# Kernel optimization log

Measured on AMD Instinct MI355X. Metric: run time of the kernel, lower is better.

## Reference

```python
import jax, jax.numpy as jnp
import numpy as np

NB_HEAD = 8
SIZE_PER_HEAD = 32
KEY_SIZE = 32
RATE = 2


def extract_seq_patches(x, kernel_size, rate):
    # x: [B, N, d] -> [B, N, kernel_size, d], dilated local windows (stride=rate)
    B, N, d = x.shape
    k_size = kernel_size + (rate - 1) * (kernel_size - 1)
    p_right = (k_size - 1) // 2
    p_left = k_size - 1 - p_right
    xp = jnp.pad(x, ((0, 0), (p_left, p_right), (0, 0)))
    xs = [xp[:, i:i + N] for i in range(0, k_size, rate)]  # kernel_size slices
    return jnp.stack(xs, axis=2)


def setup_inputs() -> dict:
    key = jax.random.key(0)
    k1, k2, k3 = jax.random.split(key, 3)
    B, S, D = 4, 2046, 256
    x = jax.random.normal(k1, (B, S, D), dtype=jnp.float32)
    # scale like nn.Linear init so softmax logits are well-conditioned
    W = jax.random.normal(k2, (D, NB_HEAD * SIZE_PER_HEAD), dtype=jnp.float32) / np.sqrt(D)
    b = jax.random.normal(k3, (NB_HEAD * SIZE_PER_HEAD,), dtype=jnp.float32) * 0.01
    return {"x": x, "W": W, "b": b}


def reference(x, W, b):
    rate, heads, dk, dv = RATE, NB_HEAD, KEY_SIZE, SIZE_PER_HEAD
    B, S, D = x.shape
    pad_len = rate - S % rate
    xp = jnp.pad(x, ((0, 0), (0, pad_len), (0, 0)))
    N = S + pad_len
    m = N // rate
    qkv = xp @ W + b                 # same Linear used for Q, K, V in the original
    Q = K = V = qkv                  # [B, N, heads*dk]
    ksz = 1 + 2 * (rate - 1)
    kwp = extract_seq_patches(K, ksz, rate)   # [B, N, ksz, H*dk]
    vwp = extract_seq_patches(V, ksz, rate)
    qw = Q.reshape(B, m, rate, heads, dk).transpose(0, 3, 2, 1, 4)   # [B,H,r,m,dk]
    kw = K.reshape(B, m, rate, heads, dk).transpose(0, 3, 2, 1, 4)
    vw = V.reshape(B, m, rate, heads, dv).transpose(0, 3, 2, 1, 4)
    kwp = kwp.reshape(B, m, rate, ksz, heads, dk).transpose(0, 4, 2, 1, 3, 5)  # [B,H,r,m,ksz,dk]
    vwp = vwp.reshape(B, m, rate, ksz, heads, dv).transpose(0, 4, 2, 1, 3, 5)
    scale = 1.0 / np.sqrt(dk).astype(np.float32)
    # strided scores; original transposes the last two dims (a.permute(0,1,2,4,3))
    a = jnp.einsum('bhrid,bhrjd->bhrji', qw, kw) * scale             # [B,H,r,m,m]
    # local-window scores: qw (as length-1 query) against dilated patches
    ap = jnp.einsum('bhrid,bhrikd->bhrik', qw, kwp) * scale          # [B,H,r,m,ksz]
    A = jax.nn.softmax(jnp.concatenate([a, ap], axis=-1), axis=-1)
    a, ap = A[..., :m], A[..., m:]
    o1 = jnp.einsum('bhrij,bhrjd->bhrid', a, vw)                     # [B,H,r,m,dv]
    o2 = jnp.einsum('bhrik,bhrikd->bhrid', ap, vwp)
    o = (o1 + o2).transpose(0, 3, 2, 1, 4).reshape(B, N, heads * dv)
    return o[:, :-pad_len]
```

## Files before the change

### kernel.cpp

```cpp
#include <hip/hip_runtime.h>
#include <stdint.h>
#include <stddef.h>

#define NB_HEAD 8
#define DHEAD   32
#define B_      4
#define S_      2046
#define N_      2048
#define M_      1024
#define D_      256

typedef __attribute__((ext_vector_type(8))) short short8;
typedef __attribute__((ext_vector_type(4))) float f32x4;

__device__ __forceinline__ void bf2x2(uint32_t u, float& lo, float& hi) {
    union { uint32_t i; float f; } a, b;
    a.i = u << 16;
    b.i = u & 0xffff0000u;
    lo = a.f; hi = b.f;
}
__device__ __forceinline__ float bf2f(uint16_t u) {
    union { uint32_t i; float f; } v; v.i = ((uint32_t)u) << 16; return v.f;
}
__device__ __forceinline__ uint16_t f2bf(float f) {
    union { float f; uint32_t i; } v; v.f = f;
    uint32_t u = v.i;
    u += 0x7fffu + ((u >> 16) & 1u);
    return (uint16_t)(u >> 16);
}
__device__ __forceinline__ short8 ld_frag(const uint16_t* p) {
    union { uint4 u; short8 s; } v;
    v.u = *(const uint4*)p;
    return v.s;
}
__device__ __forceinline__ void unp8(short8 v, float* f) {
    union { short8 s; uint32_t u[4]; } x; x.s = v;
    #pragma unroll
    for (int k = 0; k < 4; ++k) bf2x2(x.u[k], f[2*k], f[2*k+1]);
}
__device__ __forceinline__ uint32_t pkbf(uint32_t hi, uint32_t lo) {
    return __builtin_amdgcn_perm(hi, lo, 0x07060302u);
}

__global__ __launch_bounds__(256) void wt_kernel(
    const float* __restrict__ W, uint16_t* __restrict__ Wt)
{
    const int t  = blockIdx.x * 256 + threadIdx.x;
    const int c  = t >> 6;
    const int k0 = (t & 63) * 4;
    union { uint16_t h[4]; uint2 u; } v;
    #pragma unroll
    for (int kk = 0; kk < 4; ++kk)
        v.h[kk] = f2bf(W[(size_t)(k0 + kk) * D_ + c]);
    *(uint2*)(Wt + (size_t)c * D_ + k0) = v.u;
}

__global__ __launch_bounds__(256) void proj_kernel(
    const float* __restrict__ x, const uint16_t* __restrict__ Wt,
    const float* __restrict__ bias,
    uint16_t* __restrict__ qkv, uint16_t* __restrict__ qkvT)
{
    __shared__ uint16_t Tl[64 * 80];
    const int tid  = threadIdx.x;
    const int w    = tid >> 6;
    const int lane = tid & 63;
    const int q    = lane >> 4;
    const int n16  = lane & 15;
    const int rg   = blockIdx.x >> 2;
    const int cg   = blockIdx.x & 3;
    const int n0   = rg * 64;
    const int b    = n0 >> 11;
    const int nnb  = n0 & 2047;
    const int c0   = cg * 64;

    const f32x4 kZ = {0.f, 0.f, 0.f, 0.f};
    f32x4 acc[4];
    #pragma unroll
    for (int nt = 0; nt < 4; ++nt) acc[nt] = kZ;

    const int nrow = nnb + w * 16 + n16;
    const bool ok  = (nrow < S_);
    const float* xrow = x + ((size_t)b * S_ + (ok ? nrow : 0)) * D_;

    #pragma unroll
    for (int kc = 0; kc < 8; ++kc) {
        short8 A;
        if (ok) {
            const uint32_t* xp2 = (const uint32_t*)(xrow + kc * 32 + q * 8);
            uint4 f0 = *(const uint4*)xp2;
            uint4 f1 = *(const uint4*)(xp2 + 4);
            union { uint32_t u[4]; short8 s; } av;
            av.u[0] = pkbf(f0.y + 0x8000u, f0.x + 0x8000u);
            av.u[1] = pkbf(f0.w + 0x8000u, f0.z + 0x8000u);
            av.u[2] = pkbf(f1.y + 0x8000u, f1.x + 0x8000u);
            av.u[3] = pkbf(f1.w + 0x8000u, f1.z + 0x8000u);
            A = av.s;
        } else {
            A = short8{0,0,0,0,0,0,0,0};
        }
        #pragma unroll
        for (int nt = 0; nt < 4; ++nt) {
            short8 Bf = ld_frag(Wt + (size_t)(c0 + nt * 16 + n16) * D_ + kc * 32 + q * 8);
            acc[nt] = __builtin_amdgcn_mfma_f32_16x16x32_bf16(A, Bf, acc[nt], 0, 0, 0);
        }
    }

    #pragma unroll
    for (int nt = 0; nt < 4; ++nt) {
        const float bv = bias[c0 + nt * 16 + n16];
        #pragma unroll
        for (int r = 0; r < 4; ++r)
            Tl[(w * 16 + q * 4 + r) * 80 + nt * 16 + n16] = f2bf(acc[nt][r] + bv);
    }
    __syncthreads();

    const int hloc = w >> 1, rr = w & 1;
    const int hglob = (c0 >> 5) + hloc;
    const int pglob = (b * NB_HEAD + hglob) * 2 + rr;
    const int ibase = nnb >> 1;
    uint16_t* qk = qkv  + (size_t)pglob * (M_ * DHEAD);
    uint16_t* qt = qkvT + (size_t)pglob * (M_ * DHEAD);

    {
        const int ii = lane >> 1, d0 = (lane & 1) * 16;
        const uint4* src = (const uint4*)(Tl + (2 * ii + rr) * 80 + hloc * 32 + d0);
        uint4 v0 = src[0], v1 = src[1];
        uint4* dst = (uint4*)(qk + (size_t)(ibase + ii) * DHEAD + d0);
        dst[0] = v0; dst[1] = v1;
    }
    {
        const int d = lane >> 1, ph = (lane & 1) * 16;
        uint32_t pk[8];
        #pragma unroll
        for (int t = 0; t < 16; ++t) {
            const int pos = ph + t;
            const int il = (((pos >> 2) & 1) << 4) | (((pos >> 3) & 3) << 2) | (pos & 3);
            const uint32_t vv = Tl[(2 * il + rr) * 80 + hloc * 32 + d];
            if (t & 1) pk[t >> 1] |= vv << 16; else pk[t >> 1] = vv;
        }
        uint4* dst = (uint4*)(qt + (size_t)d * M_ + ibase + ph);
        dst[0] = *(uint4*)&pk[0];
        dst[1] = *(uint4*)&pk[4];
    }
}

__global__ __launch_bounds__(256) void attn_kernel(
    const uint16_t* __restrict__ qkv, const uint16_t* __restrict__ qkvT,
    float* __restrict__ out)
{
    const float SCL = 0.17677669529663687f * 1.4426950408889634f;
    const int tid  = threadIdx.x;
    const int w    = tid >> 6;
    const int lane = tid & 63;
    const int q    = lane >> 4;
    const int n16  = lane & 15;
    const int bid  = blockIdx.x;
    const int p     = ((bid & 7) << 3) | ((bid >> 3) & 7);
    const int chunk = bid >> 6;
    const uint16_t* Xp = qkv  + (size_t)p * (M_ * DHEAD);
    const uint16_t* Xt = qkvT + (size_t)p * (M_ * DHEAD);

    const int rbase = chunk * 128 + w * 32;
    const f32x4 kZ = {0.f, 0.f, 0.f, 0.f};

    short8 Q0 = ld_frag(Xp + (size_t)(rbase + n16) * DHEAD + q * 8);
    short8 Q1 = ld_frag(Xp + (size_t)(rbase + 16 + n16) * DHEAD + q * 8);

    f32x4 Ot[2][2];
    #pragma unroll
    for (int it = 0; it < 2; ++it) { Ot[it][0] = kZ; Ot[it][1] = kZ; }
    float Lp[2] = {0.f, 0.f};

    short8 Bf[4], XF[2][2];
    #pragma unroll
    for (int g = 0; g < 4; ++g)
        Bf[g] = ld_frag(Xp + (size_t)(g * 16 + n16) * DHEAD + q * 8);
    #pragma unroll
    for (int h = 0; h < 2; ++h)
        #pragma unroll
        for (int c = 0; c < 2; ++c)
            XF[h][c] = ld_frag(Xt + (size_t)(h * 16 + n16) * M_ + c * 32 + q * 8);

    for (int tile = 0; tile < 16; ++tile) {
        f32x4 S0[4], S1[4];
        #pragma unroll
        for (int g = 0; g < 4; ++g) {
            S0[g] = __builtin_amdgcn_mfma_f32_16x16x32_bf16(Bf[g], Q0, kZ, 0, 0, 0);
            S1[g] = __builtin_amdgcn_mfma_f32_16x16x32_bf16(Bf[g], Q1, kZ, 0, 0, 0);
        }
        const int jb2 = ((tile + 1) & 15) * 64;
        short8 Bn[4], XFn[2][2];
        #pragma unroll
        for (int g = 0; g < 4; ++g)
            Bn[g] = ld_frag(Xp + (size_t)(jb2 + g * 16 + n16) * DHEAD + q * 8);
        #pragma unroll
        for (int h = 0; h < 2; ++h)
            #pragma unroll
            for (int c = 0; c < 2; ++c)
                XFn[h][c] = ld_frag(Xt + (size_t)(h * 16 + n16) * M_ + jb2 + c * 32 + q * 8);

        #pragma unroll
        for (int it = 0; it < 2; ++it) {
            f32x4* S = it ? S1 : S0;
            uint32_t t[4][4];
            float rs = 0.f;
            #pragma unroll
            for (int g = 0; g < 4; ++g)
                #pragma unroll
                for (int r = 0; r < 4; ++r) {
                    float e = exp2f(S[g][r] * SCL);
                    uint32_t tt = (__float_as_uint(e) + 0x8000u) & 0xffff0000u;
                    t[g][r] = tt;
                    rs += __uint_as_float(tt);
                }
            Lp[it] += rs;
            #pragma unroll
            for (int c = 0; c < 2; ++c) {
                union { uint32_t u[4]; short8 s; } bp;
                bp.u[0] = pkbf(t[2*c][1],   t[2*c][0]);
                bp.u[1] = pkbf(t[2*c][3],   t[2*c][2]);
                bp.u[2] = pkbf(t[2*c+1][1], t[2*c+1][0]);
                bp.u[3] = pkbf(t[2*c+1][3], t[2*c+1][2]);
                Ot[it][0] = __builtin_amdgcn_mfma_f32_16x16x32_bf16(XF[0][c], bp.s, Ot[it][0], 0, 0, 0);
                Ot[it][1] = __builtin_amdgcn_mfma_f32_16x16x32_bf16(XF[1][c], bp.s, Ot[it][1], 0, 0, 0);
            }
        }
        #pragma unroll
        for (int g = 0; g < 4; ++g) Bf[g] = Bn[g];
        #pragma unroll
        for (int h = 0; h < 2; ++h) {
            XF[h][0] = XFn[h][0]; XF[h][1] = XFn[h][1];
        }
    }

    #pragma unroll
    for (int it = 0; it < 2; ++it) {
        Lp[it] += __shfl_xor(Lp[it], 16, 64);
        Lp[it] += __shfl_xor(Lp[it], 32, 64);
    }

    const int rpar  = p & 1;
    const int hh    = (p >> 1) & 7;
    const int bglob = p >> 4;

    #pragma unroll
    for (int it = 0; it < 2; ++it) {
        const int i = rbase + it * 16 + n16;
        float qf[8];
        unp8(it ? Q1 : Q0, qf);
        const int im1 = max(i - 1, 0);
        const int ip1 = min(i + 1, M_ - 1);

        float fm[8], fp[8];
        unp8(ld_frag(Xp + (size_t)im1 * DHEAD + q * 8), fm);
        unp8(ld_frag(Xp + (size_t)ip1 * DHEAD + q * 8), fp);
        float sm = 0.f, s0 = 0.f, sp = 0.f;
        #pragma unroll
        for (int jj = 0; jj < 8; ++jj) {
            sm = fmaf(qf[jj], fm[jj], sm);
            s0 = fmaf(qf[jj], qf[jj], s0);
            sp = fmaf(qf[jj], fp[jj], sp);
        }
        sm += __shfl_xor(sm, 16, 64); sm += __shfl_xor(sm, 32, 64);
        s0 += __shfl_xor(s0, 16, 64); s0 += __shfl_xor(s0, 32, 64);
        sp += __shfl_xor(sp, 16, 64); sp += __shfl_xor(sp, 32, 64);

        const bool vOK = (i > 0), wOK = (i < M_ - 1);
        const float em = vOK ? exp2f(sm * SCL) : 1.0f;
        const float e0 = exp2f(s0 * SCL);
        const float ep = wOK ? exp2f(sp * SCL) : 1.0f;
        const float vm = vOK ? em : 0.f;
        const float vp = wOK ? ep : 0.f;
        const float inv = 1.0f / (Lp[it] + em + e0 + ep);

        if (i < M_ - 1) {
            const size_t rowb = ((size_t)bglob * S_ + 2 * i + rpar) * D_ + hh * DHEAD;
            #pragma unroll
            for (int h = 0; h < 2; ++h) {
                float xm[4], x0[4], xp4[4];
                {
                    uint2 u = *(const uint2*)(Xp + (size_t)im1 * DHEAD + h * 16 + q * 4);
                    bf2x2(u.x, xm[0], xm[1]); bf2x2(u.y, xm[2], xm[3]);
                }
                {
                    uint2 u = *(const uint2*)(Xp + (size_t)i * DHEAD + h * 16 + q * 4);
                    bf2x2(u.x, x0[0], x0[1]); bf2x2(u.y, x0[2], x0[3]);
                }
                {
                    uint2 u = *(const uint2*)(Xp + (size_t)ip1 * DHEAD + h * 16 + q * 4);
                    bf2x2(u.x, xp4[0], xp4[1]); bf2x2(u.y, xp4[2], xp4[3]);
                }
                float4 res;
                #pragma unroll
                for (int r = 0; r < 4; ++r) {
                    float v = Ot[it][h][r] + vm * xm[r] + e0 * x0[r] + vp * xp4[r];
                    ((float*)&res)[r] = v * inv;
                }
                *(float4*)(out + rowb + h * 16 + q * 4) = res;
            }
        }
    }
}

extern "C" void kernel_launch(void* const* d_in, const int* in_sizes, int n_in,
                              void* d_out, int out_size, void* d_ws, size_t ws_size,
                              hipStream_t stream) {
    const float* x    = (const float*)d_in[0];
    const float* W    = (const float*)d_in[1];
    const float* bias = (const float*)d_in[2];
    uint16_t* qkv  = (uint16_t*)d_ws;
    uint16_t* qkvT = (uint16_t*)d_ws + (size_t)64 * M_ * DHEAD;
    uint16_t* Wt   = qkvT + (size_t)64 * M_ * DHEAD;
    float* out = (float*)d_out;

    hipLaunchKernelGGL(wt_kernel,   dim3(64),  dim3(256), 0, stream, W, Wt);
    hipLaunchKernelGGL(proj_kernel, dim3(512), dim3(256), 0, stream,
                       x, Wt, bias, qkv, qkvT);
    hipLaunchKernelGGL(attn_kernel, dim3(512), dim3(256), 0, stream,
                       qkv, qkvT, out);
}
```

Before: 106.9 us.

## Halve per-block work in projection and attention kernels to double grid size

```diff
diff --git a/kernel.cpp b/kernel.cpp
--- a/kernel.cpp
+++ b/kernel.cpp
@@ -60,23 +60,22 @@
     const float* __restrict__ bias,
     uint16_t* __restrict__ qkv, uint16_t* __restrict__ qkvT)
 {
-    __shared__ uint16_t Tl[64 * 80];
+    __shared__ uint16_t Tl[64 * 40];
     const int tid  = threadIdx.x;
     const int w    = tid >> 6;
     const int lane = tid & 63;
     const int q    = lane >> 4;
     const int n16  = lane & 15;
-    const int rg   = blockIdx.x >> 2;
-    const int cg   = blockIdx.x & 3;
+    const int rg   = blockIdx.x >> 3;
+    const int cg   = blockIdx.x & 7;
     const int n0   = rg * 64;
     const int b    = n0 >> 11;
     const int nnb  = n0 & 2047;
-    const int c0   = cg * 64;
+    const int c0   = cg * 32;
 
     const f32x4 kZ = {0.f, 0.f, 0.f, 0.f};
-    f32x4 acc[4];
-    #pragma unroll
-    for (int nt = 0; nt < 4; ++nt) acc[nt] = kZ;
+    f32x4 acc[2];
+    acc[0] = kZ; acc[1] = kZ;
 
     const int nrow = nnb + w * 16 + n16;
     const bool ok  = (nrow < S_);
@@ -99,48 +98,46 @@
             A = short8{0,0,0,0,0,0,0,0};
         }
         #pragma unroll
-        for (int nt = 0; nt < 4; ++nt) {
+        for (int nt = 0; nt < 2; ++nt) {
             short8 Bf = ld_frag(Wt + (size_t)(c0 + nt * 16 + n16) * D_ + kc * 32 + q * 8);
             acc[nt] = __builtin_amdgcn_mfma_f32_16x16x32_bf16(A, Bf, acc[nt], 0, 0, 0);
         }
     }
 
     #pragma unroll
-    for (int nt = 0; nt < 4; ++nt) {
+    for (int nt = 0; nt < 2; ++nt) {
         const float bv = bias[c0 + nt * 16 + n16];
         #pragma unroll
         for (int r = 0; r < 4; ++r)
-            Tl[(w * 16 + q * 4 + r) * 80 + nt * 16 + n16] = f2bf(acc[nt][r] + bv);
+            Tl[(w * 16 + q * 4 + r) * 40 + nt * 16 + n16] = f2bf(acc[nt][r] + bv);
     }
     __syncthreads();
 
-    const int hloc = w >> 1, rr = w & 1;
-    const int hglob = (c0 >> 5) + hloc;
-    const int pglob = (b * NB_HEAD + hglob) * 2 + rr;
+    const int rr   = w & 1;
+    const int half = w >> 1;
+    const int pglob = (b * NB_HEAD + cg) * 2 + rr;
     const int ibase = nnb >> 1;
     uint16_t* qk = qkv  + (size_t)pglob * (M_ * DHEAD);
     uint16_t* qt = qkvT + (size_t)pglob * (M_ * DHEAD);
 
     {
-        const int ii = lane >> 1, d0 = (lane & 1) * 16;
-        const uint4* src = (const uint4*)(Tl + (2 * ii + rr) * 80 + hloc * 32 + d0);
-        uint4 v0 = src[0], v1 = src[1];
-        uint4* dst = (uint4*)(qk + (size_t)(ibase + ii) * DHEAD + d0);
-        dst[0] = v0; dst[1] = v1;
+        const int il = half * 16 + (lane >> 2);
+        const int d0 = (lane & 3) * 8;
+        uint4 v = *(const uint4*)(Tl + (2 * il + rr) * 40 + d0);
+        *(uint4*)(qk + (size_t)(ibase + il) * DHEAD + d0) = v;
     }
     {
-        const int d = lane >> 1, ph = (lane & 1) * 16;
-        uint32_t pk[8];
-        #pragma unroll
-        for (int t = 0; t < 16; ++t) {
-            const int pos = ph + t;
+        const int d  = half * 16 + (lane >> 2);
+        const int p0 = (lane & 3) * 8;
+        uint32_t pk[4];
+        #pragma unroll
+        for (int t = 0; t < 8; ++t) {
+            const int pos = p0 + t;
             const int il = (((pos >> 2) & 1) << 4) | (((pos >> 3) & 3) << 2) | (pos & 3);
-            const uint32_t vv = Tl[(2 * il + rr) * 80 + hloc * 32 + d];
+            const uint32_t vv = Tl[(2 * il + rr) * 40 + d];
             if (t & 1) pk[t >> 1] |= vv << 16; else pk[t >> 1] = vv;
         }
-        uint4* dst = (uint4*)(qt + (size_t)d * M_ + ibase + ph);
-        dst[0] = *(uint4*)&pk[0];
-        dst[1] = *(uint4*)&pk[4];
+        *(uint4*)(qt + (size_t)d * M_ + ibase + p0) = *(uint4*)&pk[0];
     }
 }
 
@@ -160,16 +157,14 @@
     const uint16_t* Xp = qkv  + (size_t)p * (M_ * DHEAD);
     const uint16_t* Xt = qkvT + (size_t)p * (M_ * DHEAD);
 
-    const int rbase = chunk * 128 + w * 32;
+    const int rbase = chunk * 64 + w * 16;
     const f32x4 kZ = {0.f, 0.f, 0.f, 0.f};
 
     short8 Q0 = ld_frag(Xp + (size_t)(rbase + n16) * DHEAD + q * 8);
-    short8 Q1 = ld_frag(Xp + (size_t)(rbase + 16 + n16) * DHEAD + q * 8);
-
-    f32x4 Ot[2][2];
-    #pragma unroll
-    for (int it = 0; it < 2; ++it) { Ot[it][0] = kZ; Ot[it][1] = kZ; }
-    float Lp[2] = {0.f, 0.f};
+
+    f32x4 Ot[2];
+    Ot[0] = kZ; Ot[1] = kZ;
+    float Lp = 0.f;
 
     short8 Bf[4], XF[2][2];
     #pragma unroll
@@ -182,12 +177,11 @@
             XF[h][c] = ld_frag(Xt + (size_t)(h * 16 + n16) * M_ + c * 32 + q * 8);
 
     for (int tile = 0; tile < 16; ++tile) {
-        f32x4 S0[4], S1[4];
-        #pragma unroll
-        for (int g = 0; g < 4; ++g) {
-            S0[g] = __builtin_amdgcn_mfma_f32_16x16x32_bf16(Bf[g], Q0, kZ, 0, 0, 0);
-            S1[g] = __builtin_amdgcn_mfma_f32_16x16x32_bf16(Bf[g], Q1, kZ, 0, 0, 0);
-        }
+        f32x4 S[4];
+        #pragma unroll
+        for (int g = 0; g < 4; ++g)
+            S[g] = __builtin_amdgcn_mfma_f32_16x16x32_bf16(Bf[g], Q0, kZ, 0, 0, 0);
+
         const int jb2 = ((tile + 1) & 15) * 64;
         short8 Bn[4], XFn[2][2];
         #pragma unroll
@@ -199,31 +193,26 @@
             for (int c = 0; c < 2; ++c)
                 XFn[h][c] = ld_frag(Xt + (size_t)(h * 16 + n16) * M_ + jb2 + c * 32 + q * 8);
 
-        #pragma unroll
-        for (int it = 0; it < 2; ++it) {
-            f32x4* S = it ? S1 : S0;
-            uint32_t t[4][4];
-            float rs = 0.f;
+        uint32_t t[4][4];
+        float rs = 0.f;
+        #pragma unroll
+        for (int g = 0; g < 4; ++g)
             #pragma unroll
-            for (int g = 0; g < 4; ++g)
-                #pragma unroll
-                for (int r = 0; r < 4; ++r) {
-                    float e = exp2f(S[g][r] * SCL);
-                    uint32_t tt = (__float_as_uint(e) + 0x8000u) & 0xffff0000u;
-                    t[g][r] = tt;
-                    rs += __uint_as_float(tt);
-                }
-            Lp[it] += rs;
-            #pragma unroll
-            for (int c = 0; c < 2; ++c) {
-                union { uint32_t u[4]; short8 s; } bp;
-                bp.u[0] = pkbf(t[2*c][1],   t[2*c][0]);
-                bp.u[1] = pkbf(t[2*c][3],   t[2*c][2]);
-                bp.u[2] = pkbf(t[2*c+1][1], t[2*c+1][0]);
-                bp.u[3] = pkbf(t[2*c+1][3], t[2*c+1][2]);
-                Ot[it][0] = __builtin_amdgcn_mfma_f32_16x16x32_bf16(XF[0][c], bp.s, Ot[it][0], 0, 0, 0);
-                Ot[it][1] = __builtin_amdgcn_mfma_f32_16x16x32_bf16(XF[1][c], bp.s, Ot[it][1], 0, 0, 0);
+            for (int r = 0; r < 4; ++r) {
+                float e = exp2f(S[g][r] * SCL);
+                t[g][r] = __float_as_uint(e) + 0x8000u;
+                rs += e;
             }
+        Lp += rs;
+        #pragma unroll
+        for (int c = 0; c < 2; ++c) {
+            union { uint32_t u[4]; short8 s; } bp;
+            bp.u[0] = pkbf(t[2*c][1],   t[2*c][0]);
+            bp.u[1] = pkbf(t[2*c][3],   t[2*c][2]);
+            bp.u[2] = pkbf(t[2*c+1][1], t[2*c+1][0]);
+            bp.u[3] = pkbf(t[2*c+1][3], t[2*c+1][2]);
+            Ot[0] = __builtin_amdgcn_mfma_f32_16x16x32_bf16(XF[0][c], bp.s, Ot[0], 0, 0, 0);
+            Ot[1] = __builtin_amdgcn_mfma_f32_16x16x32_bf16(XF[1][c], bp.s, Ot[1], 0, 0, 0);
         }
         #pragma unroll
         for (int g = 0; g < 4; ++g) Bf[g] = Bn[g];
@@ -233,21 +222,17 @@
         }
     }
 
-    #pragma unroll
-    for (int it = 0; it < 2; ++it) {
-        Lp[it] += __shfl_xor(Lp[it], 16, 64);
-        Lp[it] += __shfl_xor(Lp[it], 32, 64);
-    }
+    Lp += __shfl_xor(Lp, 16, 64);
+    Lp += __shfl_xor(Lp, 32, 64);
 
     const int rpar  = p & 1;
     const int hh    = (p >> 1) & 7;
     const int bglob = p >> 4;
 
-    #pragma unroll
-    for (int it = 0; it < 2; ++it) {
-        const int i = rbase + it * 16 + n16;
+    {
+        const int i = rbase + n16;
         float qf[8];
-        unp8(it ? Q1 : Q0, qf);
+        unp8(Q0, qf);
         const int im1 = max(i - 1, 0);
         const int ip1 = min(i + 1, M_ - 1);
 
@@ -271,7 +256,7 @@
         const float ep = wOK ? exp2f(sp * SCL) : 1.0f;
         const float vm = vOK ? em : 0.f;
         const float vp = wOK ? ep : 0.f;
-        const float inv = 1.0f / (Lp[it] + em + e0 + ep);
+        const float inv = 1.0f / (Lp + em + e0 + ep);
 
         if (i < M_ - 1) {
             const size_t rowb = ((size_t)bglob * S_ + 2 * i + rpar) * D_ + hh * DHEAD;
@@ -293,7 +278,7 @@
                 float4 res;
                 #pragma unroll
                 for (int r = 0; r < 4; ++r) {
-                    float v = Ot[it][h][r] + vm * xm[r] + e0 * x0[r] + vp * xp4[r];
+                    float v = Ot[h][r] + vm * xm[r] + e0 * x0[r] + vp * xp4[r];
                     ((float*)&res)[r] = v * inv;
                 }
                 *(float4*)(out + rowb + h * 16 + q * 4) = res;
@@ -313,9 +298,9 @@
     uint16_t* Wt   = qkvT + (size_t)64 * M_ * DHEAD;
     float* out = (float*)d_out;
 
-    hipLaunchKernelGGL(wt_kernel,   dim3(64),  dim3(256), 0, stream, W, Wt);
-    hipLaunchKernelGGL(proj_kernel, dim3(512), dim3(256), 0, stream,
+    hipLaunchKernelGGL(wt_kernel,   dim3(64),   dim3(256), 0, stream, W, Wt);
+    hipLaunchKernelGGL(proj_kernel, dim3(1024), dim3(256), 0, stream,
                        x, Wt, bias, qkv, qkvT);
-    hipLaunchKernelGGL(attn_kernel, dim3(512), dim3(256), 0, stream,
+    hipLaunchKernelGGL(attn_kernel, dim3(1024), dim3(256), 0, stream,
                        qkv, qkvT, out);
 }
```

New measurement: 140.8 us. 1.32x slower.

## Split reduction dimension across two wave groups in projection and attention kernels

Applied to the files above, without the earlier changes.

```diff
diff --git a/kernel.cpp b/kernel.cpp
--- a/kernel.cpp
+++ b/kernel.cpp
@@ -55,17 +55,20 @@
     *(uint2*)(Wt + (size_t)c * D_ + k0) = v.u;
 }
 
-__global__ __launch_bounds__(256) void proj_kernel(
+__global__ __launch_bounds__(512) void proj_kernel(
     const float* __restrict__ x, const uint16_t* __restrict__ Wt,
     const float* __restrict__ bias,
     uint16_t* __restrict__ qkv, uint16_t* __restrict__ qkvT)
 {
+    __shared__ float    mrgP[4][16][64];
     __shared__ uint16_t Tl[64 * 80];
     const int tid  = threadIdx.x;
     const int w    = tid >> 6;
     const int lane = tid & 63;
     const int q    = lane >> 4;
     const int n16  = lane & 15;
+    const int rp   = w & 3;
+    const int kh   = w >> 2;
     const int rg   = blockIdx.x >> 2;
     const int cg   = blockIdx.x & 3;
     const int n0   = rg * 64;
@@ -78,15 +81,16 @@
     #pragma unroll
     for (int nt = 0; nt < 4; ++nt) acc[nt] = kZ;
 
-    const int nrow = nnb + w * 16 + n16;
+    const int nrow = nnb + rp * 16 + n16;
     const bool ok  = (nrow < S_);
     const float* xrow = x + ((size_t)b * S_ + (ok ? nrow : 0)) * D_;
 
     #pragma unroll
-    for (int kc = 0; kc < 8; ++kc) {
+    for (int kc = 0; kc < 4; ++kc) {
+        const int k0 = kh * 128 + kc * 32;
         short8 A;
         if (ok) {
-            const uint32_t* xp2 = (const uint32_t*)(xrow + kc * 32 + q * 8);
+            const uint32_t* xp2 = (const uint32_t*)(xrow + k0 + q * 8);
             uint4 f0 = *(const uint4*)xp2;
             uint4 f1 = *(const uint4*)(xp2 + 4);
             union { uint32_t u[4]; short8 s; } av;
@@ -100,67 +104,85 @@
         }
         #pragma unroll
         for (int nt = 0; nt < 4; ++nt) {
-            short8 Bf = ld_frag(Wt + (size_t)(c0 + nt * 16 + n16) * D_ + kc * 32 + q * 8);
+            short8 Bf = ld_frag(Wt + (size_t)(c0 + nt * 16 + n16) * D_ + k0 + q * 8);
             acc[nt] = __builtin_amdgcn_mfma_f32_16x16x32_bf16(A, Bf, acc[nt], 0, 0, 0);
         }
     }
 
-    #pragma unroll
-    for (int nt = 0; nt < 4; ++nt) {
-        const float bv = bias[c0 + nt * 16 + n16];
-        #pragma unroll
-        for (int r = 0; r < 4; ++r)
-            Tl[(w * 16 + q * 4 + r) * 80 + nt * 16 + n16] = f2bf(acc[nt][r] + bv);
+    if (kh == 1) {
+        #pragma unroll
+        for (int nt = 0; nt < 4; ++nt)
+            #pragma unroll
+            for (int r = 0; r < 4; ++r)
+                mrgP[rp][nt * 4 + r][lane] = acc[nt][r];
     }
     __syncthreads();
-
-    const int hloc = w >> 1, rr = w & 1;
-    const int hglob = (c0 >> 5) + hloc;
-    const int pglob = (b * NB_HEAD + hglob) * 2 + rr;
-    const int ibase = nnb >> 1;
-    uint16_t* qk = qkv  + (size_t)pglob * (M_ * DHEAD);
-    uint16_t* qt = qkvT + (size_t)pglob * (M_ * DHEAD);
-
-    {
-        const int ii = lane >> 1, d0 = (lane & 1) * 16;
-        const uint4* src = (const uint4*)(Tl + (2 * ii + rr) * 80 + hloc * 32 + d0);
-        uint4 v0 = src[0], v1 = src[1];
-        uint4* dst = (uint4*)(qk + (size_t)(ibase + ii) * DHEAD + d0);
-        dst[0] = v0; dst[1] = v1;
-    }
-    {
-        const int d = lane >> 1, ph = (lane & 1) * 16;
-        uint32_t pk[8];
-        #pragma unroll
-        for (int t = 0; t < 16; ++t) {
-            const int pos = ph + t;
-            const int il = (((pos >> 2) & 1) << 4) | (((pos >> 3) & 3) << 2) | (pos & 3);
-            const uint32_t vv = Tl[(2 * il + rr) * 80 + hloc * 32 + d];
-            if (t & 1) pk[t >> 1] |= vv << 16; else pk[t >> 1] = vv;
-        }
-        uint4* dst = (uint4*)(qt + (size_t)d * M_ + ibase + ph);
-        dst[0] = *(uint4*)&pk[0];
-        dst[1] = *(uint4*)&pk[4];
-    }
-}
-
-__global__ __launch_bounds__(256) void attn_kernel(
+    if (kh == 0) {
+        #pragma unroll
+        for (int nt = 0; nt < 4; ++nt) {
+            const float bv = bias[c0 + nt * 16 + n16];
+            #pragma unroll
+            for (int r = 0; r < 4; ++r) {
+                float v = acc[nt][r] + mrgP[rp][nt * 4 + r][lane] + bv;
+                Tl[(rp * 16 + q * 4 + r) * 80 + nt * 16 + n16] = f2bf(v);
+            }
+        }
+    }
+    __syncthreads();
+
+    if (w < 4) {
+        const int hloc = w >> 1, rr = w & 1;
+        const int hglob = (c0 >> 5) + hloc;
+        const int pglob = (b * NB_HEAD + hglob) * 2 + rr;
+        const int ibase = nnb >> 1;
+        uint16_t* qk = qkv  + (size_t)pglob * (M_ * DHEAD);
+        uint16_t* qt = qkvT + (size_t)pglob * (M_ * DHEAD);
+
+        {
+            const int ii = lane >> 1, d0 = (lane & 1) * 16;
+            const uint4* src = (const uint4*)(Tl + (2 * ii + rr) * 80 + hloc * 32 + d0);
+            uint4 v0 = src[0], v1 = src[1];
+            uint4* dst = (uint4*)(qk + (size_t)(ibase + ii) * DHEAD + d0);
+            dst[0] = v0; dst[1] = v1;
+        }
+        {
+            const int d = lane >> 1, ph = (lane & 1) * 16;
+            uint32_t pk[8];
+            #pragma unroll
+            for (int t = 0; t < 16; ++t) {
+                const int pos = ph + t;
+                const int il = (((pos >> 2) & 1) << 4) | (((pos >> 3) & 3) << 2) | (pos & 3);
+                const uint32_t vv = Tl[(2 * il + rr) * 80 + hloc * 32 + d];
+                if (t & 1) pk[t >> 1] |= vv << 16; else pk[t >> 1] = vv;
+            }
+            uint4* dst = (uint4*)(qt + (size_t)d * M_ + ibase + ph);
+            dst[0] = *(uint4*)&pk[0];
+            dst[1] = *(uint4*)&pk[4];
+        }
+    }
+}
+
+__global__ __launch_bounds__(512) void attn_kernel(
     const uint16_t* __restrict__ qkv, const uint16_t* __restrict__ qkvT,
     float* __restrict__ out)
 {
     const float SCL = 0.17677669529663687f * 1.4426950408889634f;
+    __shared__ float mrg[4][18][64];
     const int tid  = threadIdx.x;
     const int w    = tid >> 6;
     const int lane = tid & 63;
     const int q    = lane >> 4;
     const int n16  = lane & 15;
+    const int rowgrp = w & 3;
+    const int jh     = w >> 2;
     const int bid  = blockIdx.x;
     const int p     = ((bid & 7) << 3) | ((bid >> 3) & 7);
     const int chunk = bid >> 6;
     const uint16_t* Xp = qkv  + (size_t)p * (M_ * DHEAD);
     const uint16_t* Xt = qkvT + (size_t)p * (M_ * DHEAD);
 
-    const int rbase = chunk * 128 + w * 32;
+    const int rbase = chunk * 128 + rowgrp * 32;
+    const int jb0   = jh * 512;
     const f32x4 kZ = {0.f, 0.f, 0.f, 0.f};
 
     short8 Q0 = ld_frag(Xp + (size_t)(rbase + n16) * DHEAD + q * 8);
@@ -174,21 +196,21 @@
     short8 Bf[4], XF[2][2];
     #pragma unroll
     for (int g = 0; g < 4; ++g)
-        Bf[g] = ld_frag(Xp + (size_t)(g * 16 + n16) * DHEAD + q * 8);
+        Bf[g] = ld_frag(Xp + (size_t)(jb0 + g * 16 + n16) * DHEAD + q * 8);
     #pragma unroll
     for (int h = 0; h < 2; ++h)
         #pragma unroll
         for (int c = 0; c < 2; ++c)
-            XF[h][c] = ld_frag(Xt + (size_t)(h * 16 + n16) * M_ + c * 32 + q * 8);
-
-    for (int tile = 0; tile < 16; ++tile) {
+            XF[h][c] = ld_frag(Xt + (size_t)(h * 16 + n16) * M_ + jb0 + c * 32 + q * 8);
+
+    for (int tile = 0; tile < 8; ++tile) {
         f32x4 S0[4], S1[4];
         #pragma unroll
         for (int g = 0; g < 4; ++g) {
             S0[g] = __builtin_amdgcn_mfma_f32_16x16x32_bf16(Bf[g], Q0, kZ, 0, 0, 0);
             S1[g] = __builtin_amdgcn_mfma_f32_16x16x32_bf16(Bf[g], Q1, kZ, 0, 0, 0);
         }
-        const int jb2 = ((tile + 1) & 15) * 64;
+        const int jb2 = jb0 + ((tile + 1) & 7) * 64;
         short8 Bn[4], XFn[2][2];
         #pragma unroll
         for (int g = 0; g < 4; ++g)
@@ -237,6 +259,30 @@
     for (int it = 0; it < 2; ++it) {
         Lp[it] += __shfl_xor(Lp[it], 16, 64);
         Lp[it] += __shfl_xor(Lp[it], 32, 64);
+    }
+
+    if (jh == 1) {
+        #pragma unroll
+        for (int it = 0; it < 2; ++it)
+            #pragma unroll
+            for (int h = 0; h < 2; ++h)
+                #pragma unroll
+                for (int r = 0; r < 4; ++r)
+                    mrg[rowgrp][it * 8 + h * 4 + r][lane] = Ot[it][h][r];
+        mrg[rowgrp][16][lane] = Lp[0];
+        mrg[rowgrp][17][lane] = Lp[1];
+    }
+    __syncthreads();
+    if (jh == 1) return;
+
+    #pragma unroll
+    for (int it = 0; it < 2; ++it) {
+        #pragma unroll
+        for (int h = 0; h < 2; ++h)
+            #pragma unroll
+            for (int r = 0; r < 4; ++r)
+                Ot[it][h][r] += mrg[rowgrp][it * 8 + h * 4 + r][lane];
+        Lp[it] += mrg[rowgrp][16 + it][lane];
     }
 
     const int rpar  = p & 1;
@@ -314,8 +360,8 @@
     float* out = (float*)d_out;
 
     hipLaunchKernelGGL(wt_kernel,   dim3(64),  dim3(256), 0, stream, W, Wt);
-    hipLaunchKernelGGL(proj_kernel, dim3(512), dim3(256), 0, stream,
+    hipLaunchKernelGGL(proj_kernel, dim3(512), dim3(512), 0, stream,
                        x, Wt, bias, qkv, qkvT);
-    hipLaunchKernelGGL(attn_kernel, dim3(512), dim3(256), 0, stream,
+    hipLaunchKernelGGL(attn_kernel, dim3(512), dim3(512), 0, stream,
                        qkv, qkvT, out);
 }
```

Result: no change. 106.5 us (-0.4%).
